# Kernel tuning notes

Measured on AMD Instinct MI355X. Metric: run time of the kernel, lower is better.

The kernel has to match this reference:

```python
import jax, jax.numpy as jnp
import numpy as np

B, S, K = 8, 1024, 4


def setup_inputs() -> dict:
    key = jax.random.key(0)
    ks = jax.random.split(key, 12)
    inp = {
        "aspect_logits": jax.random.normal(ks[0], (B, S, 4), jnp.float32),
        "opinion_logits": jax.random.normal(ks[1], (B, S, 4), jnp.float32),
        "aspect_opinion_relations": jax.random.uniform(ks[2], (B, S, S, K), jnp.float32),
        "explicit_aspects": jax.random.randint(ks[3], (B, S), 0, 2, jnp.int64),
        "explicit_opinions": jax.random.randint(ks[4], (B, S), 0, 2, jnp.int64),
        # aspect_opinion_consistency MLP params (torch Linear(8,32)->(32,16)->(16,1))
        "W1": jax.random.normal(ks[5], (8, 32), jnp.float32) * 0.35,
        "b1": jnp.zeros((32,), jnp.float32),
        "W2": jax.random.normal(ks[6], (32, 16), jnp.float32) * 0.18,
        "b2": jnp.zeros((16,), jnp.float32),
        "W3": jax.random.normal(ks[7], (16, 1), jnp.float32) * 0.25,
        "b3": jnp.zeros((1,), jnp.float32),
    }
    return inp


def _window_any(flag, w):
    # flag: [B, S] bool -> any within +-w positions (inclusive)
    s = flag.shape[1]
    p = jnp.pad(flag, ((0, 0), (w, w)))
    return jnp.any(jnp.stack([p[:, k:k + s] for k in range(2 * w + 1)], 0), axis=0)


def _forward(aL, oL, rel, exA, exO, W1, b1, W2, b2, W3, b3):
    bsz, slen, _ = aL.shape
    # --- step 1: consistency MLP factor (applied to full rows) ---
    x = jnp.concatenate([aL, oL], axis=-1)  # [B,S,8]
    h = jax.nn.relu(x @ W1 + b1)
    h = jax.nn.relu(h @ W2 + b2)
    c = jax.nn.sigmoid(h @ W3 + b3)[..., 0]  # [B,S]
    # if c < 0.5: row *= 1 - (0.5 - c)*2 == 2c
    mult1 = jnp.where(c < 0.5, 2.0 * c, 1.0)

    # --- step 2: implicit requires nearby explicit (window 3) ---
    nearA = _window_any(exA > 0, 3)
    nearO = _window_any(exO > 0, 3)
    impA = jax.nn.softmax(aL, axis=-1)[..., :2].sum(-1)
    impO = jax.nn.softmax(oL, axis=-1)[..., :2].sum(-1)
    factA2 = jnp.where((impA > 0.5) & ~nearO, 0.3, 1.0)
    factO2 = jnp.where((impO > 0.5) & ~nearA, 0.3, 1.0)

    # --- step 4: causality ordering (relation to an earlier opinion position) ---
    rel_any = jnp.any(rel > 0.5, axis=-1)            # [B,S,S] (i, opinion pos p)
    maxrel = jnp.max(rel, axis=(-2, -1))             # [B,S]
    earlier = jnp.tril(jnp.ones((slen, slen), bool), k=-1)  # earlier[i,p]: p < i
    exists_earlier = jnp.any(rel_any & earlier[None], axis=-1)
    factA4 = jnp.where((maxrel > 0.5) & exists_earlier, 0.7, 1.0)

    # --- step 3: isolation check reads partially-updated constrained arrays ->
    # genuine sequential dependency over seq positions -> lax.scan ---
    idx = jnp.arange(slen)

    def step(carry, i):
        cA, cO = carry
        act = (cA.max(-1) > 0.5) | (cO.max(-1) > 0.5)     # [B,S]
        wmask = (jnp.abs(idx - i) <= 2) & (idx != i)       # window 2, exclude self
        isolated = ~jnp.any(act & wmask[None], axis=1)     # [B]
        fact3 = jnp.where(isolated, 0.1, 1.0)
        aRow = aL[:, i] * mult1[:, i, None]
        oRow = oL[:, i] * mult1[:, i, None]
        fa = factA2[:, i] * fact3 * factA4[:, i]
        fo = factO2[:, i] * fact3
        aRow = aRow.at[:, :2].multiply(fa[:, None])
        oRow = oRow.at[:, :2].multiply(fo[:, None])
        return (cA.at[:, i].set(aRow), cO.at[:, i].set(oRow)), None

    (cA, cO), _ = jax.lax.scan(step, (aL, oL), idx)
    return cA, cO


def reference(aspect_logits, opinion_logits, aspect_opinion_relations,
              explicit_aspects, explicit_opinions, W1, b1, W2, b2, W3, b3):
    return _forward(aspect_logits, opinion_logits, aspect_opinion_relations,
                    explicit_aspects, explicit_opinions, W1, b1, W2, b2, W3, b3)
```

## Files before the change

### kernel.cpp

```cpp
#include <hip/hip_runtime.h>
#include <cstdint>
#include <cmath>

#define SEQ 1024
#define BATCH 8
#define NK 4

__global__ __launch_bounds__(256) void krelA(const float* __restrict__ rel,
                                             float* __restrict__ factA4) {
    int row = blockIdx.x;
    int i = row & (SEQ - 1);
    const float4* row4 = reinterpret_cast<const float4*>(rel) + (size_t)row * SEQ;
    int tid = threadIdx.x;
    bool found = false;
    for (int base = 0; base < i; base += 256) {
        int p = base + tid;
        bool pred = false;
        if (p < i) {
            float4 v = row4[p];
            pred = (v.x > 0.5f) | (v.y > 0.5f) | (v.z > 0.5f) | (v.w > 0.5f);
        }
        if (__syncthreads_or((int)pred)) { found = true; break; }
    }
    if (tid == 0) factA4[row] = found ? 0.7f : 1.0f;
}

__global__ __launch_bounds__(256) void kfact(
    const float4* __restrict__ aL4, const float4* __restrict__ oL4,
    const int* __restrict__ exA, const int* __restrict__ exO,
    const float* __restrict__ W1, const float* __restrict__ b1,
    const float* __restrict__ W2, const float* __restrict__ b2,
    const float* __restrict__ W3, const float* __restrict__ b3,
    const float* __restrict__ factA4,
    float* __restrict__ mult1_o, float* __restrict__ faf_o,
    float* __restrict__ fof_o, int* __restrict__ flags_o) {
    int gid = blockIdx.x * 256 + threadIdx.x;
    int b = gid >> 10, i = gid & (SEQ - 1);

    float4 a = aL4[gid], o = oL4[gid];
    float x[8] = {a.x, a.y, a.z, a.w, o.x, o.y, o.z, o.w};

    float h1[32];
#pragma unroll
    for (int j = 0; j < 32; ++j) h1[j] = b1[j];
#pragma unroll
    for (int k = 0; k < 8; ++k)
#pragma unroll
        for (int j = 0; j < 32; ++j) h1[j] = fmaf(x[k], W1[k * 32 + j], h1[j]);
#pragma unroll
    for (int j = 0; j < 32; ++j) h1[j] = fmaxf(h1[j], 0.0f);

    float h2[16];
#pragma unroll
    for (int j = 0; j < 16; ++j) h2[j] = b2[j];
#pragma unroll
    for (int k = 0; k < 32; ++k)
#pragma unroll
        for (int j = 0; j < 16; ++j) h2[j] = fmaf(h1[k], W2[k * 16 + j], h2[j]);
#pragma unroll
    for (int j = 0; j < 16; ++j) h2[j] = fmaxf(h2[j], 0.0f);

    float z = b3[0];
#pragma unroll
    for (int k = 0; k < 16; ++k) z = fmaf(h2[k], W3[k], z);
    float c = 1.0f / (1.0f + expf(-z));
    float m1 = (c < 0.5f) ? (2.0f * c) : 1.0f;

    float ma = fmaxf(fmaxf(a.x, a.y), fmaxf(a.z, a.w));
    float ea0 = expf(a.x - ma), ea1 = expf(a.y - ma), ea2 = expf(a.z - ma), ea3 = expf(a.w - ma);
    bool impA = (ea0 + ea1) / (ea0 + ea1 + ea2 + ea3) > 0.5f;
    float mo = fmaxf(fmaxf(o.x, o.y), fmaxf(o.z, o.w));
    float eo0 = expf(o.x - mo), eo1 = expf(o.y - mo), eo2 = expf(o.z - mo), eo3 = expf(o.w - mo);
    bool impO = (eo0 + eo1) / (eo0 + eo1 + eo2 + eo3) > 0.5f;

    bool nearA = false, nearO = false;
#pragma unroll
    for (int d = -3; d <= 3; ++d) {
        int j = i + d;
        if (j >= 0 && j < SEQ) {
            nearA |= exA[b * SEQ + j] > 0;
            nearO |= exO[b * SEQ + j] > 0;
        }
    }
    float fA2 = (impA && !nearO) ? 0.3f : 1.0f;
    float fO2 = (impO && !nearA) ? 0.3f : 1.0f;
    float faf = fA2 * factA4[gid];
    float fof = fO2;

    float a01 = fmaxf(a.x, a.y) * m1, a23 = fmaxf(a.z, a.w) * m1;
    float o01 = fmaxf(o.x, o.y) * m1, o23 = fmaxf(o.z, o.w) * m1;
    bool actNon = (fmaxf(a01 * faf, a23) > 0.5f) || (fmaxf(o01 * fof, o23) > 0.5f);
    bool actIso = (fmaxf(a01 * faf * 0.1f, a23) > 0.5f) || (fmaxf(o01 * fof * 0.1f, o23) > 0.5f);
    bool actOrig = (ma > 0.5f) || (mo > 0.5f);

    mult1_o[gid] = m1;
    faf_o[gid] = faf;
    fof_o[gid] = fof;
    flags_o[gid] = (int)actIso | ((int)actNon << 1) | ((int)actOrig << 2);
}

__global__ __launch_bounds__(256) void kapply(
    const float4* __restrict__ aL4, const float4* __restrict__ oL4,
    const float* __restrict__ mult1, const float* __restrict__ faf,
    const float* __restrict__ fof, const int* __restrict__ flags,
    float4* __restrict__ outA4, float4* __restrict__ outO4) {
    int b = blockIdx.x;
    int tid = threadIdx.x;
    int base = b * SEQ;
    __shared__ unsigned long long A64[16], N64[16], R64[16], ISO[16];

#pragma unroll
    for (int it = 0; it < 4; ++it) {
        int pos = it * 256 + tid;
        int f  = flags[base + pos];
        int f1 = (pos + 1 < SEQ) ? flags[base + pos + 1] : 0;
        int f2 = (pos + 2 < SEQ) ? flags[base + pos + 2] : 0;
        int rbit = ((f1 >> 2) | (f2 >> 2)) & 1;
        unsigned long long bA = __ballot(f & 1);
        unsigned long long bN = __ballot((f >> 1) & 1);
        unsigned long long bR = __ballot(rbit);
        int w = it * 4 + (tid >> 6);
        if ((tid & 63) == 0) { A64[w] = bA; N64[w] = bN; R64[w] = bR; }
    }
    __syncthreads();

    if (tid == 0) {
        unsigned int u1 = 0, u2 = 0;
        for (int w = 0; w < 16; ++w) {
            unsigned long long aw = A64[w], nw = N64[w], rw = R64[w];
            unsigned long long isoW = 0;
#pragma unroll
            for (int j = 0; j < 64; ++j) {
                unsigned int ro  = (unsigned int)(rw >> j) & 1u;
                unsigned int iso = (u1 | u2 | ro) ^ 1u;
                unsigned int ab  = (unsigned int)(aw >> j) & 1u;
                unsigned int nb  = (unsigned int)(nw >> j) & 1u;
                unsigned int u   = iso ? ab : nb;
                isoW |= (unsigned long long)iso << j;
                u2 = u1; u1 = u;
            }
            ISO[w] = isoW;
        }
    }
    __syncthreads();

#pragma unroll
    for (int it = 0; it < 4; ++it) {
        int pos = it * 256 + tid;
        int gid = base + pos;
        unsigned int iso = (unsigned int)(ISO[pos >> 6] >> (pos & 63)) & 1u;
        float f3 = iso ? 0.1f : 1.0f;
        float m  = mult1[gid];
        float fa = faf[gid] * f3;
        float fo = fof[gid] * f3;
        float4 a = aL4[gid], o = oL4[gid];
        float4 ra  = make_float4(a.x * m * fa, a.y * m * fa, a.z * m, a.w * m);
        float4 rt  = make_float4(o.x * m * fo, o.y * m * fo, o.z * m, o.w * m);
        outA4[gid] = ra;
        outO4[gid] = rt;
    }
}

extern "C" void kernel_launch(void* const* d_in, const int* in_sizes, int n_in,
                              void* d_out, int out_size, void* d_ws, size_t ws_size,
                              hipStream_t stream) {
    const float* aL  = (const float*)d_in[0];
    const float* oL  = (const float*)d_in[1];
    const float* rel = (const float*)d_in[2];
    const int*   exA = (const int*)d_in[3];
    const int*   exO = (const int*)d_in[4];
    const float* W1 = (const float*)d_in[5];
    const float* b1 = (const float*)d_in[6];
    const float* W2 = (const float*)d_in[7];
    const float* b2 = (const float*)d_in[8];
    const float* W3 = (const float*)d_in[9];
    const float* b3 = (const float*)d_in[10];

    float* ws     = (float*)d_ws;
    float* factA4 = ws;
    float* mult1  = ws + 8192;
    float* faf    = ws + 16384;
    float* fof    = ws + 24576;
    int*   flags  = (int*)(ws + 32768);

    float* out = (float*)d_out;

    krelA<<<BATCH * SEQ, 256, 0, stream>>>(rel, factA4);
    kfact<<<(BATCH * SEQ) / 256, 256, 0, stream>>>(
        (const float4*)aL, (const float4*)oL, exA, exO,
        W1, b1, W2, b2, W3, b3, factA4, mult1, faf, fof, flags);
    kapply<<<BATCH, 256, 0, stream>>>(
        (const float4*)aL, (const float4*)oL, mult1, faf, fof, flags,
        (float4*)out, (float4*)(out + (size_t)BATCH * SEQ * NK));
}
```

Before: 231.5 us.

## Fuse factor and apply kernels, use wave-per-row relation scan

The MLP/factor kernel and the sequential isolation-apply kernel are merged into one kernel with one 1024-thread block per batch, so intermediates stay in registers instead of going through workspace, and one launch is removed. The relation scan now gives each 64-lane wavefront its own row and uses a wave-wide any instead of a block-wide barrier, which cuts synchronisation and lets rows exit early independently. The isolation recurrence is also rewritten with simpler boolean logic and shifted ballot masks. The trade-off is that the fused kernel runs only 8 blocks, each carrying the full MLP register footprint at 1024 threads.

```diff
diff --git a/kernel.cpp b/kernel.cpp
--- a/kernel.cpp
+++ b/kernel.cpp
@@ -8,34 +8,36 @@
 
 __global__ __launch_bounds__(256) void krelA(const float* __restrict__ rel,
                                              float* __restrict__ factA4) {
-    int row = blockIdx.x;
+    int row  = blockIdx.x * 4 + (threadIdx.x >> 6);
+    int lane = threadIdx.x & 63;
     int i = row & (SEQ - 1);
     const float4* row4 = reinterpret_cast<const float4*>(rel) + (size_t)row * SEQ;
-    int tid = threadIdx.x;
     bool found = false;
-    for (int base = 0; base < i; base += 256) {
-        int p = base + tid;
+    for (int base = 0; base < i; base += 64) {
+        int p = base + lane;
         bool pred = false;
         if (p < i) {
             float4 v = row4[p];
             pred = (v.x > 0.5f) | (v.y > 0.5f) | (v.z > 0.5f) | (v.w > 0.5f);
         }
-        if (__syncthreads_or((int)pred)) { found = true; break; }
+        if (__any((int)pred)) { found = true; break; }
     }
-    if (tid == 0) factA4[row] = found ? 0.7f : 1.0f;
+    if (lane == 0) factA4[row] = found ? 0.7f : 1.0f;
 }
 
-__global__ __launch_bounds__(256) void kfact(
+__global__ __launch_bounds__(1024) void kfused(
     const float4* __restrict__ aL4, const float4* __restrict__ oL4,
     const int* __restrict__ exA, const int* __restrict__ exO,
     const float* __restrict__ W1, const float* __restrict__ b1,
     const float* __restrict__ W2, const float* __restrict__ b2,
     const float* __restrict__ W3, const float* __restrict__ b3,
     const float* __restrict__ factA4,
-    float* __restrict__ mult1_o, float* __restrict__ faf_o,
-    float* __restrict__ fof_o, int* __restrict__ flags_o) {
-    int gid = blockIdx.x * 256 + threadIdx.x;
-    int b = gid >> 10, i = gid & (SEQ - 1);
+    float4* __restrict__ outA4, float4* __restrict__ outO4) {
+    int b = blockIdx.x;
+    int pos = threadIdx.x;
+    int gid = b * SEQ + pos;
+
+    __shared__ unsigned long long A64[16], N64[16], O64[16], ISO[16];
 
     float4 a = aL4[gid], o = oL4[gid];
     float x[8] = {a.x, a.y, a.z, a.w, o.x, o.y, o.z, o.w};
@@ -76,7 +78,7 @@
     bool nearA = false, nearO = false;
 #pragma unroll
     for (int d = -3; d <= 3; ++d) {
-        int j = i + d;
+        int j = pos + d;
         if (j >= 0 && j < SEQ) {
             nearA |= exA[b * SEQ + j] > 0;
             nearO |= exO[b * SEQ + j] > 0;
@@ -93,72 +95,42 @@
     bool actIso = (fmaxf(a01 * faf * 0.1f, a23) > 0.5f) || (fmaxf(o01 * fof * 0.1f, o23) > 0.5f);
     bool actOrig = (ma > 0.5f) || (mo > 0.5f);
 
-    mult1_o[gid] = m1;
-    faf_o[gid] = faf;
-    fof_o[gid] = fof;
-    flags_o[gid] = (int)actIso | ((int)actNon << 1) | ((int)actOrig << 2);
-}
-
-__global__ __launch_bounds__(256) void kapply(
-    const float4* __restrict__ aL4, const float4* __restrict__ oL4,
-    const float* __restrict__ mult1, const float* __restrict__ faf,
-    const float* __restrict__ fof, const int* __restrict__ flags,
-    float4* __restrict__ outA4, float4* __restrict__ outO4) {
-    int b = blockIdx.x;
-    int tid = threadIdx.x;
-    int base = b * SEQ;
-    __shared__ unsigned long long A64[16], N64[16], R64[16], ISO[16];
-
-#pragma unroll
-    for (int it = 0; it < 4; ++it) {
-        int pos = it * 256 + tid;
-        int f  = flags[base + pos];
-        int f1 = (pos + 1 < SEQ) ? flags[base + pos + 1] : 0;
-        int f2 = (pos + 2 < SEQ) ? flags[base + pos + 2] : 0;
-        int rbit = ((f1 >> 2) | (f2 >> 2)) & 1;
-        unsigned long long bA = __ballot(f & 1);
-        unsigned long long bN = __ballot((f >> 1) & 1);
-        unsigned long long bR = __ballot(rbit);
-        int w = it * 4 + (tid >> 6);
-        if ((tid & 63) == 0) { A64[w] = bA; N64[w] = bN; R64[w] = bR; }
-    }
+    unsigned long long bA = __ballot((int)actIso);
+    unsigned long long bN = __ballot((int)actNon);
+    unsigned long long bO = __ballot((int)actOrig);
+    int w = pos >> 6;
+    if ((pos & 63) == 0) { A64[w] = bA; N64[w] = bN; O64[w] = bO; }
     __syncthreads();
 
-    if (tid == 0) {
+    if (pos == 0) {
         unsigned int u1 = 0, u2 = 0;
-        for (int w = 0; w < 16; ++w) {
-            unsigned long long aw = A64[w], nw = N64[w], rw = R64[w];
+        for (int wi = 0; wi < 16; ++wi) {
+            unsigned long long aw = A64[wi], nw = N64[wi];
+            unsigned long long ow = O64[wi];
+            unsigned long long on = (wi < 15) ? O64[wi + 1] : 0ull;
+            unsigned long long rw = ((ow >> 1) | (on << 63)) | ((ow >> 2) | (on << 62));
             unsigned long long isoW = 0;
 #pragma unroll
             for (int j = 0; j < 64; ++j) {
-                unsigned int ro  = (unsigned int)(rw >> j) & 1u;
-                unsigned int iso = (u1 | u2 | ro) ^ 1u;
-                unsigned int ab  = (unsigned int)(aw >> j) & 1u;
-                unsigned int nb  = (unsigned int)(nw >> j) & 1u;
-                unsigned int u   = iso ? ab : nb;
-                isoW |= (unsigned long long)iso << j;
+                unsigned int ro = (unsigned int)(rw >> j) & 1u;
+                unsigned int t  = u1 | u2 | ro;
+                unsigned int ab = (unsigned int)(aw >> j) & 1u;
+                unsigned int nb = (unsigned int)(nw >> j) & 1u;
+                unsigned int u  = ab | (nb & t);
+                isoW |= (unsigned long long)(t ^ 1u) << j;
                 u2 = u1; u1 = u;
             }
-            ISO[w] = isoW;
+            ISO[wi] = isoW;
         }
     }
     __syncthreads();
 
-#pragma unroll
-    for (int it = 0; it < 4; ++it) {
-        int pos = it * 256 + tid;
-        int gid = base + pos;
-        unsigned int iso = (unsigned int)(ISO[pos >> 6] >> (pos & 63)) & 1u;
-        float f3 = iso ? 0.1f : 1.0f;
-        float m  = mult1[gid];
-        float fa = faf[gid] * f3;
-        float fo = fof[gid] * f3;
-        float4 a = aL4[gid], o = oL4[gid];
-        float4 ra  = make_float4(a.x * m * fa, a.y * m * fa, a.z * m, a.w * m);
-        float4 rt  = make_float4(o.x * m * fo, o.y * m * fo, o.z * m, o.w * m);
-        outA4[gid] = ra;
-        outO4[gid] = rt;
-    }
+    unsigned int iso = (unsigned int)(ISO[pos >> 6] >> (pos & 63)) & 1u;
+    float f3 = iso ? 0.1f : 1.0f;
+    float fa = faf * f3;
+    float fo = fof * f3;
+    outA4[gid] = make_float4(a.x * m1 * fa, a.y * m1 * fa, a.z * m1, a.w * m1);
+    outO4[gid] = make_float4(o.x * m1 * fo, o.y * m1 * fo, o.z * m1, o.w * m1);
 }
 
 extern "C" void kernel_launch(void* const* d_in, const int* in_sizes, int n_in,
@@ -176,20 +148,12 @@
     const float* W3 = (const float*)d_in[9];
     const float* b3 = (const float*)d_in[10];
 
-    float* ws     = (float*)d_ws;
-    float* factA4 = ws;
-    float* mult1  = ws + 8192;
-    float* faf    = ws + 16384;
-    float* fof    = ws + 24576;
-    int*   flags  = (int*)(ws + 32768);
-
+    float* factA4 = (float*)d_ws;
     float* out = (float*)d_out;
 
-    krelA<<<BATCH * SEQ, 256, 0, stream>>>(rel, factA4);
-    kfact<<<(BATCH * SEQ) / 256, 256, 0, stream>>>(
+    krelA<<<(BATCH * SEQ) / 4, 256, 0, stream>>>(rel, factA4);
+    kfused<<<BATCH, 1024, 0, stream>>>(
         (const float4*)aL, (const float4*)oL, exA, exO,
-        W1, b1, W2, b2, W3, b3, factA4, mult1, faf, fof, flags);
-    kapply<<<BATCH, 256, 0, stream>>>(
-        (const float4*)aL, (const float4*)oL, mult1, faf, fof, flags,
+        W1, b1, W2, b2, W3, b3, factA4,
         (float4*)out, (float4*)(out + (size_t)BATCH * SEQ * NK));
 }
```

Result: no change. 234.0 us (+1.1%).
